# Optimization experiments

Hardware: AMD Instinct MI355X
Metric: run time of the kernel (lower is better)

Reference implementation:

```python
import jax, jax.numpy as jnp
import numpy as np

N_NODES = 100000
N_EDGES = 3200000


def setup_inputs() -> dict:
    key = jax.random.key(0)
    ks = jax.random.split(key, 12)
    x = jax.random.normal(ks[0], (N_NODES, 5), dtype=jnp.float32)
    edges = jax.random.randint(ks[1], (2, N_EDGES), 0, N_NODES)
    edge_attr = jax.random.normal(ks[2], (N_EDGES, 2), dtype=jnp.float32)
    detector_labels = jax.random.bernoulli(ks[3], 0.7, (N_NODES,))

    def init(k, shape, fan_in):
        return (jax.random.normal(k, shape, dtype=jnp.float32) / np.sqrt(fan_in)).astype(jnp.float32)

    W_gat = init(ks[4], (5, 16), 5)        # GATConv lin (shared src/dst)
    att_src = init(ks[5], (16,), 16)
    att_dst = init(ks[6], (16,), 16)
    W_edge = init(ks[7], (2, 16), 2)       # GATConv lin_edge
    att_edge = init(ks[8], (16,), 16)
    b_gat = jnp.zeros((16,), jnp.float32)
    W1 = init(ks[9], (34, 64), 34)
    b1 = jnp.zeros((64,), jnp.float32)
    W2 = init(ks[10], (64, 2), 64)
    b2 = jnp.zeros((2,), jnp.float32)
    return dict(x=x, edges=edges, edge_attr=edge_attr, detector_labels=detector_labels,
                W_gat=W_gat, att_src=att_src, att_dst=att_dst, W_edge=W_edge,
                att_edge=att_edge, b_gat=b_gat, W1=W1, b1=b1, W2=W2, b2=b2)


def reference(x, edges, edge_attr, detector_labels, W_gat, att_src, att_dst,
              W_edge, att_edge, b_gat, W1, b1, W2, b2):
    n_nodes = x.shape[0]
    src, dst = edges[0], edges[1]

    # --- GATConv(5 -> 16, heads=1, concat=False, edge_dim=2, no self loops) ---
    h = x @ W_gat                                        # [N, 16]
    a_src = h @ att_src                                  # [N]
    a_dst = h @ att_dst                                  # [N]
    a_edge = (edge_attr @ W_edge) @ att_edge             # [E]
    alpha = jax.nn.leaky_relu(a_src[src] + a_dst[dst] + a_edge, 0.2)
    # segmented softmax over incoming edges of each dst node
    seg_max = jax.ops.segment_max(alpha, dst, num_segments=n_nodes)
    ex = jnp.exp(alpha - seg_max[dst])
    denom = jax.ops.segment_sum(ex, dst, num_segments=n_nodes)
    a = ex / (denom[dst] + 1e-16)                        # [E]
    out = jax.ops.segment_sum(h[src] * a[:, None], dst, num_segments=n_nodes) + b_gat
    xh = jax.nn.relu(out)                                # [N, 16]

    # --- edge update: gather-concat-MLP ---
    feat = jnp.concatenate([xh[src], edge_attr, xh[dst]], axis=-1)   # [E, 34]
    ef = jax.nn.relu(feat @ W1 + b1) @ W2 + b2                       # [E, 2]

    # --- SplitSyndromes: keep edges whose both endpoints are detectors ---
    valid = detector_labels[src] & detector_labels[dst]
    idx = jnp.nonzero(valid)[0]        # eager (data-dependent size, not jitted)
    return edges[:, idx], jax.nn.sigmoid(ef[idx])
```

## Files before the change

### kernel.cpp

```cpp
#include <hip/hip_runtime.h>

#define NN 100000
#define NE 3200000
#define CH 8192
#define NCB ((NE + CH - 1) / CH)
#define THR 1024
#define ITH (CH / THR)
#define NBK ((NN + 63) >> 6)
#define CAP 2560
#define NWG (NE / 64)
#define NSTRIP 8
#define SLEN ((NCB + NSTRIP - 1) / NSTRIP)

typedef __attribute__((ext_vector_type(8))) __bf16 bf16x8;
typedef __attribute__((ext_vector_type(4))) float f32x4;

union BF8 { unsigned short u[8]; bf16x8 v; };

__global__ void kdetect(const unsigned char* __restrict__ lab8, int* __restrict__ flags) {
  __shared__ int tmp[256];
  int t = threadIdx.x;
  int s = 0;
  for (int i = t; i < 25000; i += 256) s += lab8[4 * i + 1];
  tmp[t] = s;
  __syncthreads();
  for (int d = 128; d > 0; d >>= 1) { if (t < d) tmp[t] += tmp[t + d]; __syncthreads(); }
  if (t == 0) flags[0] = (tmp[0] != 0) ? 1 : 0;
}

__global__ void klab(const void* __restrict__ lab, const int* __restrict__ flags,
                     int* __restrict__ labN) {
  int n = blockIdx.x * 256 + threadIdx.x;
  if (n >= NN) return;
  int v;
  if (flags[0]) v = ((const unsigned char*)lab)[n];
  else          v = ((const int*)lab)[n];
  labN[n] = (v != 0) ? 1 : 0;
}

__global__ void kc01(const float* __restrict__ We, const float* __restrict__ ae,
                     float* __restrict__ c01) {
  if (threadIdx.x == 0) {
    float c0 = 0.f, c1 = 0.f;
    for (int k = 0; k < 16; k++) { c0 += We[k] * ae[k]; c1 += We[16 + k] * ae[k]; }
    c01[0] = c0; c01[1] = c1;
  }
}

__global__ void knodeA(const float* __restrict__ x, const float* __restrict__ Wg,
                       const float* __restrict__ atts, const float* __restrict__ attd,
                       const int* __restrict__ labN,
                       float2* __restrict__ pka, float2* __restrict__ pkd) {
  int n = blockIdx.x * 256 + threadIdx.x;
  if (n >= NN) return;
  float xi[5];
#pragma unroll
  for (int i = 0; i < 5; i++) xi[i] = x[n * 5 + i];
  float asum = 0.f, dsum = 0.f;
#pragma unroll
  for (int k = 0; k < 16; k++) {
    float acc = 0.f;
#pragma unroll
    for (int i = 0; i < 5; i++) acc += xi[i] * Wg[i * 16 + k];
    asum += acc * atts[k];
    dsum += acc * attd[k];
  }
  float lab = labN[n] ? 1.f : 0.f;
  pka[n] = make_float2(asum, lab);
  pkd[n] = make_float2(dsum, lab);
}

__global__ __launch_bounds__(THR) void khist(const int* __restrict__ src,
                                             const int* __restrict__ dst,
                                             const int* __restrict__ labN,
                                             int* __restrict__ blkcnt,
                                             int* __restrict__ cntw,
                                             int* __restrict__ cntc) {
  __shared__ int hist[NBK];
  __shared__ int vsum;
  int tid = threadIdx.x, b = blockIdx.x;
  for (int i = tid; i < NBK; i += THR) hist[i] = 0;
  if (tid == 0) vsum = 0;
  __syncthreads();
  int lane = tid & 63, wid = tid >> 6;
  int wsum = 0;
  for (int it = 0; it < ITH; ++it) {
    int e = b * CH + it * THR + tid;
    int v = 0;
    if (e < NE) {
      int s = src[e], d = dst[e];
      atomicAdd(&hist[d >> 6], 1);
      v = labN[s] & labN[d];
    }
    unsigned long long m = __ballot(v != 0);
    int c = __popcll(m);
    if (lane == 0) {
      int wg = b * (CH / 64) + it * 16 + wid;
      if (wg < NWG) cntw[wg] = c;
      wsum += c;
    }
  }
  if (lane == 0) atomicAdd(&vsum, wsum);
  __syncthreads();
  int* row = blkcnt + (size_t)b * NBK;
  for (int i = tid; i < NBK; i += THR) row[i] = hist[i];
  if (tid == 0) cntc[b] = vsum;
}

__global__ __launch_bounds__(256) void kscanc1(int* __restrict__ blkcnt,
                                               int* __restrict__ ssum) {
  int i = blockIdx.x * 256 + threadIdx.x;
  int st = blockIdx.y;
  if (i >= NBK) return;
  int c0 = st * SLEN, c1 = min(c0 + SLEN, NCB);
  int run = 0;
  for (int c = c0; c < c1; c++) {
    int* p = blkcnt + (size_t)c * NBK + i;
    int v = *p;
    *p = run;
    run += v;
  }
  ssum[st * NBK + i] = run;
}

__global__ __launch_bounds__(256) void kscanc2(int* __restrict__ ssum,
                                               int* __restrict__ total) {
  int i = blockIdx.x * 256 + threadIdx.x;
  if (i >= NBK) return;
  int run = 0;
#pragma unroll
  for (int st = 0; st < NSTRIP; st++) {
    int v = ssum[st * NBK + i];
    ssum[st * NBK + i] = run;
    run += v;
  }
  total[i] = run;
}

__global__ __launch_bounds__(256) void kaddbb(int* __restrict__ ssum,
                                              const int* __restrict__ bb) {
  int i = blockIdx.x * 256 + threadIdx.x;
  if (i >= NBK) return;
  int v = bb[i];
#pragma unroll
  for (int st = 0; st < NSTRIP; st++) ssum[st * NBK + i] += v;
}

__global__ void kscan(const int* __restrict__ cnt, int* __restrict__ off, int nb) {
  __shared__ int tmp[256];
  __shared__ int carry;
  int t = threadIdx.x;
  if (t == 0) carry = 0;
  __syncthreads();
  for (int base = 0; base < nb; base += 256) {
    int i = base + t;
    int v = (i < nb) ? cnt[i] : 0;
    tmp[t] = v;
    __syncthreads();
    for (int d = 1; d < 256; d <<= 1) {
      int add = (t >= d) ? tmp[t - d] : 0;
      __syncthreads();
      tmp[t] += add;
      __syncthreads();
    }
    if (i < nb) off[i] = carry + tmp[t] - v;
    __syncthreads();
    if (t == 0) carry += tmp[255];
    __syncthreads();
  }
  if (t == 0) off[nb] = carry;
}

__global__ __launch_bounds__(128) void kscanw(const int* __restrict__ cntw,
                                              const int* __restrict__ offc,
                                              int* __restrict__ offw) {
  int b = blockIdx.x, t = threadIdx.x;
  __shared__ int a[128];
  int wg = b * 128 + t;
  int val = (wg < NWG) ? cntw[wg] : 0;
  a[t] = val;
  __syncthreads();
  for (int d = 1; d < 128; d <<= 1) {
    int x = (t >= d) ? a[t - d] : 0;
    __syncthreads();
    a[t] += x;
    __syncthreads();
  }
  if (wg < NWG) offw[wg] = offc[b] + a[t] - val;
}

__global__ __launch_bounds__(THR) void kscat(
    const int* __restrict__ src, const int* __restrict__ dst,
    const float* __restrict__ eattr,
    const float2* __restrict__ pka, const float2* __restrict__ pkd,
    const float* __restrict__ c01,
    const int* __restrict__ blkcnt, const int* __restrict__ ssum,
    const int* __restrict__ offw,
    uint2* __restrict__ bins, float* __restrict__ out,
    float2* __restrict__ eat2, int NV) {
  __shared__ uint2 pay[CH];
  __shared__ unsigned short pbk[CH];
  __shared__ int hist[2048];
  __shared__ int ps[1024];
  __shared__ int lcur[2048];
  __shared__ int goff[NBK];
  int b = blockIdx.x, tid = threadIdx.x;
  for (int i = tid; i < 2048; i += THR) hist[i] = 0;
  float c0 = c01[0], c1 = c01[1];
  const int* bc = blkcnt + (size_t)b * NBK;
  const int* ss = ssum + (size_t)(b / SLEN) * NBK;
  __syncthreads();
  int lane = tid & 63, wid = tid >> 6;
  uint2 st[ITH];
  unsigned short sb[ITH];
#pragma unroll
  for (int it = 0; it < ITH; ++it) {
    int e = b * CH + it * THR + tid;
    int v = 0;
    int s = 0, d = 0;
    float2 ea;
    if (e < NE) {
      s = src[e]; d = dst[e];
      ea = ((const float2*)eattr)[e];
      float2 ga = pka[s], gd = pkd[d];
      float al = ga.x + gd.x + ea.x * c0 + ea.y * c1;
      al = (al > 0.f) ? al : 0.2f * al;
      float exv = __expf(al);
      int bk = d >> 6;
      atomicAdd(&hist[bk], 1);
      st[it].x = ((unsigned)s << 6) | (unsigned)(d & 63);
      st[it].y = __float_as_uint(exv);
      sb[it] = (unsigned short)bk;
      v = (ga.y != 0.f) && (gd.y != 0.f);
    } else {
      sb[it] = 0xffffu;
    }
    unsigned long long m = __ballot(v);
    if (v) {
      int wg = b * (CH / 64) + it * 16 + wid;
      int p = offw[wg] + __popcll(m & ((1ull << lane) - 1ull));
      if (p < NV) {
        out[p] = (float)s;
        out[NV + p] = (float)d;
        eat2[p] = ea;
      }
    }
  }
  __syncthreads();
  int h0 = hist[2 * tid], h1 = hist[2 * tid + 1];
  ps[tid] = h0 + h1;
  __syncthreads();
  for (int d = 1; d < 1024; d <<= 1) {
    int v = (tid >= d) ? ps[tid - d] : 0;
    __syncthreads();
    ps[tid] += v;
    __syncthreads();
  }
  int epair = (tid > 0) ? ps[tid - 1] : 0;
  int l0 = epair, l1 = epair + h0;
  lcur[2 * tid] = l0;
  lcur[2 * tid + 1] = l1;
  {
    int i0 = 2 * tid, i1 = 2 * tid + 1;
    if (i0 < NBK) goff[i0] = ss[i0] + bc[i0] - l0;
    if (i1 < NBK) goff[i1] = ss[i1] + bc[i1] - l1;
  }
  __syncthreads();
#pragma unroll
  for (int it = 0; it < ITH; ++it) {
    if (sb[it] != 0xffffu) {
      int pos = atomicAdd(&lcur[sb[it]], 1);
      pay[pos] = st[it];
      pbk[pos] = sb[it];
    }
  }
  __syncthreads();
  int n = ps[1023];
  for (int j = tid; j < n; j += THR) {
    int i = pbk[j];
    bins[goff[i] + j] = pay[j];
  }
}

__global__ __launch_bounds__(512) void kagg(
    const uint2* __restrict__ bins, const int* __restrict__ bucket_base,
    const float* __restrict__ x, const float* __restrict__ Wg,
    const float* __restrict__ bg, unsigned short* __restrict__ xb) {
  __shared__ uint2 pay[CAP];
  __shared__ int cnt[64], inc[64], cur[64];
  __shared__ float sWg[80], sbg[16];
  int k = blockIdx.x, tid = threadIdx.x;
  if (tid < 80) sWg[tid] = Wg[tid];
  else if (tid < 96) sbg[tid - 80] = bg[tid - 80];
  int start = bucket_base[k], end = bucket_base[k + 1];
  int node0 = k << 6;
  int c = tid & 15, g = tid >> 4;
  __syncthreads();
  float w0 = sWg[c], w1 = sWg[16 + c], w2 = sWg[32 + c], w3 = sWg[48 + c], w4 = sWg[64 + c];
  float acc[2] = {0.f, 0.f}, den[2] = {0.f, 0.f};
  for (int cb = start; cb < end; cb += CAP) {
    int n = min(end - cb, CAP);
    if (tid < 64) cnt[tid] = 0;
    __syncthreads();
    uint2 st0, st1, st2, st3, st4;
    {
      int i;
      i = tid;          if (i < n) { st0 = bins[cb + i]; atomicAdd(&cnt[st0.x & 63], 1); }
      i = tid + 512;    if (i < n) { st1 = bins[cb + i]; atomicAdd(&cnt[st1.x & 63], 1); }
      i = tid + 1024;   if (i < n) { st2 = bins[cb + i]; atomicAdd(&cnt[st2.x & 63], 1); }
      i = tid + 1536;   if (i < n) { st3 = bins[cb + i]; atomicAdd(&cnt[st3.x & 63], 1); }
      i = tid + 2048;   if (i < n) { st4 = bins[cb + i]; atomicAdd(&cnt[st4.x & 63], 1); }
    }
    __syncthreads();
    if (tid < 64) inc[tid] = cnt[tid];
    __syncthreads();
    for (int d = 1; d < 64; d <<= 1) {
      int v = 0;
      if (tid >= d && tid < 64) v = inc[tid - d];
      __syncthreads();
      if (tid < 64) inc[tid] += v;
      __syncthreads();
    }
    if (tid < 64) cur[tid] = inc[tid] - cnt[tid];
    __syncthreads();
    {
      int i;
      i = tid;          if (i < n) pay[atomicAdd(&cur[st0.x & 63], 1)] = st0;
      i = tid + 512;    if (i < n) pay[atomicAdd(&cur[st1.x & 63], 1)] = st1;
      i = tid + 1024;   if (i < n) pay[atomicAdd(&cur[st2.x & 63], 1)] = st2;
      i = tid + 1536;   if (i < n) pay[atomicAdd(&cur[st3.x & 63], 1)] = st3;
      i = tid + 2048;   if (i < n) pay[atomicAdd(&cur[st4.x & 63], 1)] = st4;
    }
    __syncthreads();
#pragma unroll
    for (int p = 0; p < 2; ++p) {
      int nd = p * 32 + g;
      int re = inc[nd], rs = re - cnt[nd];
      float a = 0.f, ds = 0.f;
      for (int idx = rs; idx < re; ++idx) {
        uint2 pl = pay[idx];
        int s = (int)(pl.x >> 6);
        float exv = __uint_as_float(pl.y);
        const float* xp = x + s * 5;
        float h = xp[0] * w0 + xp[1] * w1 + xp[2] * w2 + xp[3] * w3 + xp[4] * w4;
        a += h * exv;
        ds += exv;
      }
      acc[p] += a; den[p] += ds;
    }
    __syncthreads();
  }
#pragma unroll
  for (int p = 0; p < 2; ++p) {
    int node = node0 + p * 32 + g;
    if (node < NN) {
      float dn = fmaxf(den[p], 1e-30f);
      float v = acc[p] / dn + sbg[c];
      float vv = (v > 0.f) ? v : 0.f;
      unsigned uv = __float_as_uint(vv);
      float rem = vv - __uint_as_float(uv & 0xffff0000u);
      xb[(size_t)node * 32 + c] = (unsigned short)(uv >> 16);
      xb[(size_t)node * 32 + 16 + c] = (unsigned short)(__float_as_uint(rem) >> 16);
    }
  }
}

__global__ __launch_bounds__(256) void kmlp(
    const float2* __restrict__ eat2, const unsigned short* __restrict__ xb,
    const float* __restrict__ W1, const float* __restrict__ b1,
    const float* __restrict__ W2, const float* __restrict__ b2,
    float* __restrict__ out, int NV) {
  int tid = threadIdx.x;
  int lane = tid & 63, wid = tid >> 6;
  int lo4 = lane & 15, q = lane >> 4;

  BF8 bh[4], bl[4];
#pragma unroll
  for (int ct = 0; ct < 4; ct++) {
    int col = ct * 16 + lo4;
#pragma unroll
    for (int i = 0; i < 8; i++) {
      int k = q * 8 + i;
      int r = (k < 16) ? k : (k + 2);
      float w = W1[r * 64 + col];
      unsigned u = __float_as_uint(w);
      float rem = w - __uint_as_float(u & 0xffff0000u);
      bh[ct].u[i] = (unsigned short)(u >> 16);
      bl[ct].u[i] = (unsigned short)(__float_as_uint(rem) >> 16);
    }
  }
  float b1v[4], w16v[4], w17v[4], w2a[4], w2b[4];
#pragma unroll
  for (int ct = 0; ct < 4; ct++) {
    int j = ct * 16 + lo4;
    b1v[ct] = b1[j];
    w16v[ct] = W1[16 * 64 + j];
    w17v[ct] = W1[17 * 64 + j];
    w2a[ct] = W2[j * 2 + 0];
    w2b[ct] = W2[j * 2 + 1];
  }
  float bias20 = b2[0], bias21 = b2[1];

  int nwaves = gridDim.x * 4;
  int ntiles = (NV + 15) >> 4;
  const int half = (q < 2) ? 0 : NV;
  const int hoff = (q & 1) * 8;
  int tb0 = blockIdx.x * 4 + wid;
  if (tb0 >= ntiles) return;

  bf16x8 ah, al;
  {
    int p = tb0 * 16 + lo4;
    int node = (p < NV) ? (int)out[half + p] : 0;
    const unsigned short* xp = xb + (size_t)node * 32 + hoff;
    ah = *(const bf16x8*)xp;
    al = *(const bf16x8*)(xp + 16);
  }
  for (int tb = tb0; tb < ntiles; tb += nwaves) {
    int base = tb * 16;
    bf16x8 ah2, al2;
    {
      int tn = tb + nwaves;
      int pn = tn * 16 + lo4;
      int noden = (tn < ntiles && pn < NV) ? (int)out[half + pn] : 0;
      const unsigned short* xpn = xb + (size_t)noden * 32 + hoff;
      ah2 = *(const bf16x8*)xpn;
      al2 = *(const bf16x8*)(xpn + 16);
    }
    float2 ea[4];
#pragma unroll
    for (int reg = 0; reg < 4; reg++) {
      int pr = base + q * 4 + reg;
      ea[reg] = (pr < NV) ? eat2[pr] : make_float2(0.f, 0.f);
    }
    f32x4 acc[4];
#pragma unroll
    for (int ct = 0; ct < 4; ct++) {
      f32x4 z = {0.f, 0.f, 0.f, 0.f};
      z = __builtin_amdgcn_mfma_f32_16x16x32_bf16(ah, bh[ct].v, z, 0, 0, 0);
      z = __builtin_amdgcn_mfma_f32_16x16x32_bf16(ah, bl[ct].v, z, 0, 0, 0);
      z = __builtin_amdgcn_mfma_f32_16x16x32_bf16(al, bh[ct].v, z, 0, 0, 0);
      acc[ct] = z;
    }
#pragma unroll
    for (int reg = 0; reg < 4; reg++) {
      int pr = base + q * 4 + reg;
      float s0 = 0.f, s1 = 0.f;
#pragma unroll
      for (int ct = 0; ct < 4; ct++) {
        float h = acc[ct][reg] + b1v[ct] + ea[reg].x * w16v[ct] + ea[reg].y * w17v[ct];
        h = fmaxf(h, 0.f);
        s0 += h * w2a[ct];
        s1 += h * w2b[ct];
      }
      float a = (lo4 & 8) ? s1 : s0;
      float g = (lo4 & 8) ? s0 : s1;
      a += __uint_as_float(__builtin_amdgcn_ds_swizzle(__float_as_uint(g), 0x201F));
      a += __uint_as_float(__builtin_amdgcn_ds_swizzle(__float_as_uint(a), 0x101F));
      a += __uint_as_float(__builtin_amdgcn_ds_swizzle(__float_as_uint(a), 0x081F));
      a += __uint_as_float(__builtin_amdgcn_ds_swizzle(__float_as_uint(a), 0x041F));
      if (pr < NV) {
        if (lo4 == 0)      out[2 * (size_t)NV + 2 * pr]     = 1.f / (1.f + __expf(-(bias20 + a)));
        else if (lo4 == 8) out[2 * (size_t)NV + 2 * pr + 1] = 1.f / (1.f + __expf(-(bias21 + a)));
      }
    }
    ah = ah2; al = al2;
  }
}

static inline size_t al64(size_t v) { return (v + 63) & ~(size_t)63; }

extern "C" void kernel_launch(void* const* d_in, const int* in_sizes, int n_in,
                              void* d_out, int out_size, void* d_ws, size_t ws_size,
                              hipStream_t stream) {
  const float* x     = (const float*)d_in[0];
  const int*   edges = (const int*)d_in[1];
  const float* eattr = (const float*)d_in[2];
  const void*  labels= d_in[3];
  const float* Wg    = (const float*)d_in[4];
  const float* atts  = (const float*)d_in[5];
  const float* attd  = (const float*)d_in[6];
  const float* We    = (const float*)d_in[7];
  const float* atte  = (const float*)d_in[8];
  const float* bg    = (const float*)d_in[9];
  const float* W1    = (const float*)d_in[10];
  const float* b1    = (const float*)d_in[11];
  const float* W2    = (const float*)d_in[12];
  const float* b2    = (const float*)d_in[13];
  float* out = (float*)d_out;
  const int NV = out_size / 4;
  const int* src = edges;
  const int* dst = edges + NE;

  char* w = (char*)d_ws;
  unsigned short* xb = (unsigned short*)w;  w += al64((size_t)NN * 64);
  uint2* bins  = (uint2*)w;   w += al64((size_t)NE * 8);
  float2* eat2 = (float2*)w;  w += al64((size_t)NV * 8);
  float2* pka  = (float2*)w;  w += al64((size_t)NN * 8);
  float2* pkd  = (float2*)w;  w += al64((size_t)NN * 8);
  int* labN    = (int*)w;     w += al64((size_t)NN * 4);
  int* blkcnt  = (int*)w;     w += al64((size_t)NCB * NBK * 4);
  int* ssum    = (int*)w;     w += al64((size_t)NSTRIP * NBK * 4);
  int* total   = (int*)w;     w += al64((size_t)NBK * 4);
  int* bb      = (int*)w;     w += al64((size_t)(NBK + 1) * 4);
  int* cntc    = (int*)w;     w += al64((size_t)NCB * 4);
  int* offc    = (int*)w;     w += al64((size_t)(NCB + 1) * 4);
  int* cntw    = (int*)w;     w += al64((size_t)NWG * 4);
  int* offw    = (int*)w;     w += al64((size_t)NWG * 4);
  float* c01   = (float*)w;   w += 64;
  int* flags   = (int*)w;     w += 64;

  kdetect<<<1, 256, 0, stream>>>((const unsigned char*)labels, flags);
  klab<<<(NN + 255) / 256, 256, 0, stream>>>(labels, flags, labN);
  kc01<<<1, 64, 0, stream>>>(We, atte, c01);
  knodeA<<<(NN + 255) / 256, 256, 0, stream>>>(x, Wg, atts, attd, labN, pka, pkd);
  khist<<<NCB, THR, 0, stream>>>(src, dst, labN, blkcnt, cntw, cntc);
  kscanc1<<<dim3((NBK + 255) / 256, NSTRIP), 256, 0, stream>>>(blkcnt, ssum);
  kscanc2<<<(NBK + 255) / 256, 256, 0, stream>>>(ssum, total);
  kscan<<<1, 256, 0, stream>>>(total, bb, NBK);
  kaddbb<<<(NBK + 255) / 256, 256, 0, stream>>>(ssum, bb);
  kscan<<<1, 256, 0, stream>>>(cntc, offc, NCB);
  kscanw<<<NCB, 128, 0, stream>>>(cntw, offc, offw);
  kscat<<<NCB, THR, 0, stream>>>(src, dst, eattr, pka, pkd, c01, blkcnt, ssum,
                                 offw, bins, out, eat2, NV);
  kagg<<<NBK, 512, 0, stream>>>(bins, bb, x, Wg, bg, xb);
  if (NV > 0)
    kmlp<<<2048, 256, 0, stream>>>(eat2, xb, W1, b1, W2, b2, out, NV);
}
```

Before: 282.6 us.

## Halve edge chunk size and replace block scans with wavefront shuffle scans

Halves the per-block edge chunk. This doubles the block count and reduces the scatter kernel's LDS footprint, which should allow more blocks per CU and better load balance across CUs. The 1024-entry LDS scan in the scatter kernel and the per-chunk warp-count scan become wavefront __shfl_up scans, cutting the number of __syncthreads. The bucket-base scan and the add-back of the base into the strip sums are fused into one kernel, removing a launch. In exchange, the per-chunk histogram matrix doubles, adding global traffic in the column-scan kernels.

Result: slower. 299.3 us (+5.9%).

```diff
diff --git a/kernel.cpp b/kernel.cpp
--- a/kernel.cpp
+++ b/kernel.cpp
@@ -2,10 +2,11 @@
 
 #define NN 100000
 #define NE 3200000
-#define CH 8192
+#define CH 4096
 #define NCB ((NE + CH - 1) / CH)
 #define THR 1024
 #define ITH (CH / THR)
+#define WGC (CH / 64)
 #define NBK ((NN + 63) >> 6)
 #define CAP 2560
 #define NWG (NE / 64)
@@ -95,7 +96,7 @@
     unsigned long long m = __ballot(v != 0);
     int c = __popcll(m);
     if (lane == 0) {
-      int wg = b * (CH / 64) + it * 16 + wid;
+      int wg = b * WGC + it * 16 + wid;
       if (wg < NWG) cntw[wg] = c;
       wsum += c;
     }
@@ -137,13 +138,35 @@
   total[i] = run;
 }
 
-__global__ __launch_bounds__(256) void kaddbb(int* __restrict__ ssum,
-                                              const int* __restrict__ bb) {
-  int i = blockIdx.x * 256 + threadIdx.x;
-  if (i >= NBK) return;
-  int v = bb[i];
-#pragma unroll
-  for (int st = 0; st < NSTRIP; st++) ssum[st * NBK + i] += v;
+__global__ void kscanbb(const int* __restrict__ cnt, int* __restrict__ bb,
+                        int* __restrict__ ssum) {
+  __shared__ int tmp[256];
+  __shared__ int carry;
+  int t = threadIdx.x;
+  if (t == 0) carry = 0;
+  __syncthreads();
+  for (int base = 0; base < NBK; base += 256) {
+    int i = base + t;
+    int v = (i < NBK) ? cnt[i] : 0;
+    tmp[t] = v;
+    __syncthreads();
+    for (int d = 1; d < 256; d <<= 1) {
+      int add = (t >= d) ? tmp[t - d] : 0;
+      __syncthreads();
+      tmp[t] += add;
+      __syncthreads();
+    }
+    if (i < NBK) {
+      int o = carry + tmp[t] - v;
+      bb[i] = o;
+#pragma unroll
+      for (int st = 0; st < NSTRIP; st++) ssum[st * NBK + i] += o;
+    }
+    __syncthreads();
+    if (t == 0) carry += tmp[255];
+    __syncthreads();
+  }
+  if (t == 0) bb[NBK] = carry;
 }
 
 __global__ void kscan(const int* __restrict__ cnt, int* __restrict__ off, int nb) {
@@ -171,22 +194,19 @@
   if (t == 0) off[nb] = carry;
 }
 
-__global__ __launch_bounds__(128) void kscanw(const int* __restrict__ cntw,
+__global__ __launch_bounds__(256) void kscanw(const int* __restrict__ cntw,
                                               const int* __restrict__ offc,
                                               int* __restrict__ offw) {
-  int b = blockIdx.x, t = threadIdx.x;
-  __shared__ int a[128];
-  int wg = b * 128 + t;
+  int wg = blockIdx.x * 256 + threadIdx.x;
+  int lane = threadIdx.x & 63;
   int val = (wg < NWG) ? cntw[wg] : 0;
-  a[t] = val;
-  __syncthreads();
-  for (int d = 1; d < 128; d <<= 1) {
-    int x = (t >= d) ? a[t - d] : 0;
-    __syncthreads();
-    a[t] += x;
-    __syncthreads();
-  }
-  if (wg < NWG) offw[wg] = offc[b] + a[t] - val;
+  int sc = val;
+#pragma unroll
+  for (int d = 1; d < 64; d <<= 1) {
+    int x = __shfl_up(sc, d, 64);
+    if (lane >= d) sc += x;
+  }
+  if (wg < NWG) offw[wg] = offc[wg >> 6] + sc - val;
 }
 
 __global__ __launch_bounds__(THR) void kscat(
@@ -200,12 +220,11 @@
     float2* __restrict__ eat2, int NV) {
   __shared__ uint2 pay[CH];
   __shared__ unsigned short pbk[CH];
-  __shared__ int hist[2048];
-  __shared__ int ps[1024];
-  __shared__ int lcur[2048];
+  __shared__ int hc[2048];
   __shared__ int goff[NBK];
+  __shared__ int wsum[17];
   int b = blockIdx.x, tid = threadIdx.x;
-  for (int i = tid; i < 2048; i += THR) hist[i] = 0;
+  for (int i = tid; i < 2048; i += THR) hc[i] = 0;
   float c0 = c01[0], c1 = c01[1];
   const int* bc = blkcnt + (size_t)b * NBK;
   const int* ss = ssum + (size_t)(b / SLEN) * NBK;
@@ -227,7 +246,7 @@
       al = (al > 0.f) ? al : 0.2f * al;
       float exv = __expf(al);
       int bk = d >> 6;
-      atomicAdd(&hist[bk], 1);
+      atomicAdd(&hc[bk], 1);
       st[it].x = ((unsigned)s << 6) | (unsigned)(d & 63);
       st[it].y = __float_as_uint(exv);
       sb[it] = (unsigned short)bk;
@@ -237,7 +256,7 @@
     }
     unsigned long long m = __ballot(v);
     if (v) {
-      int wg = b * (CH / 64) + it * 16 + wid;
+      int wg = b * WGC + it * 16 + wid;
       int p = offw[wg] + __popcll(m & ((1ull << lane) - 1ull));
       if (p < NV) {
         out[p] = (float)s;
@@ -247,35 +266,43 @@
     }
   }
   __syncthreads();
-  int h0 = hist[2 * tid], h1 = hist[2 * tid + 1];
-  ps[tid] = h0 + h1;
-  __syncthreads();
-  for (int d = 1; d < 1024; d <<= 1) {
-    int v = (tid >= d) ? ps[tid - d] : 0;
-    __syncthreads();
-    ps[tid] += v;
-    __syncthreads();
-  }
-  int epair = (tid > 0) ? ps[tid - 1] : 0;
+  int h0 = hc[2 * tid], h1 = hc[2 * tid + 1];
+  int ps = h0 + h1;
+  int sc = ps;
+#pragma unroll
+  for (int d2 = 1; d2 < 64; d2 <<= 1) {
+    int x = __shfl_up(sc, d2, 64);
+    if (lane >= d2) sc += x;
+  }
+  if (lane == 63) wsum[wid] = sc;
+  __syncthreads();
+  if (tid == 0) {
+    int run = 0;
+#pragma unroll
+    for (int wq = 0; wq < 16; wq++) { int v2 = wsum[wq]; wsum[wq] = run; run += v2; }
+    wsum[16] = run;
+  }
+  __syncthreads();
+  int epair = wsum[wid] + sc - ps;
   int l0 = epair, l1 = epair + h0;
-  lcur[2 * tid] = l0;
-  lcur[2 * tid + 1] = l1;
   {
     int i0 = 2 * tid, i1 = 2 * tid + 1;
     if (i0 < NBK) goff[i0] = ss[i0] + bc[i0] - l0;
     if (i1 < NBK) goff[i1] = ss[i1] + bc[i1] - l1;
   }
+  hc[2 * tid] = l0;
+  hc[2 * tid + 1] = l1;
   __syncthreads();
 #pragma unroll
   for (int it = 0; it < ITH; ++it) {
     if (sb[it] != 0xffffu) {
-      int pos = atomicAdd(&lcur[sb[it]], 1);
+      int pos = atomicAdd(&hc[sb[it]], 1);
       pay[pos] = st[it];
       pbk[pos] = sb[it];
     }
   }
   __syncthreads();
-  int n = ps[1023];
+  int n = wsum[16];
   for (int j = tid; j < n; j += THR) {
     int i = pbk[j];
     bins[goff[i] + j] = pay[j];
@@ -517,10 +544,9 @@
   khist<<<NCB, THR, 0, stream>>>(src, dst, labN, blkcnt, cntw, cntc);
   kscanc1<<<dim3((NBK + 255) / 256, NSTRIP), 256, 0, stream>>>(blkcnt, ssum);
   kscanc2<<<(NBK + 255) / 256, 256, 0, stream>>>(ssum, total);
-  kscan<<<1, 256, 0, stream>>>(total, bb, NBK);
-  kaddbb<<<(NBK + 255) / 256, 256, 0, stream>>>(ssum, bb);
+  kscanbb<<<1, 256, 0, stream>>>(total, bb, ssum);
   kscan<<<1, 256, 0, stream>>>(cntc, offc, NCB);
-  kscanw<<<NCB, 128, 0, stream>>>(cntw, offc, offw);
+  kscanw<<<(NWG + 255) / 256, 256, 0, stream>>>(cntw, offc, offw);
   kscat<<<NCB, THR, 0, stream>>>(src, dst, eattr, pka, pkd, c01, blkcnt, ssum,
                                  offw, bins, out, eat2, NV);
   kagg<<<NBK, 512, 0, stream>>>(bins, bb, x, Wg, bg, xb);
```
